# Kernel tuning notes

Hardware: AMD Instinct MI355X
Metric: run time of the kernel (lower is better)

The kernel has to match this reference:

```python
import jax, jax.numpy as jnp
import numpy as np

EMBED_DIM = 512
U_EMBED = 6
NUM_HEADS = 8
HEAD_DIM = EMBED_DIM // NUM_HEADS
SCALE = HEAD_DIM ** -0.5
BS, N = 8, 1024


def setup_inputs() -> dict:
    key = jax.random.key(0)
    ks = jax.random.split(key, 9)
    x = jax.random.normal(ks[0], (BS, N, EMBED_DIM), dtype=jnp.float32)
    u = jax.random.normal(ks[1], (BS, U_EMBED, N, N), dtype=jnp.float32)
    umask = jax.random.randint(ks[2], (BS, N, N, 1), 0, 2).astype(bool)
    s = EMBED_DIM ** -0.5
    Wq = jax.random.normal(ks[3], (EMBED_DIM, EMBED_DIM), dtype=jnp.float32) * s
    Wk = jax.random.normal(ks[4], (EMBED_DIM, EMBED_DIM), dtype=jnp.float32) * s
    Wv = jax.random.normal(ks[5], (EMBED_DIM, EMBED_DIM), dtype=jnp.float32) * s
    Wu = jax.random.normal(ks[6], (NUM_HEADS, U_EMBED), dtype=jnp.float32) * (U_EMBED ** -0.5)
    bu = jnp.zeros((NUM_HEADS,), dtype=jnp.float32)
    Wo = jax.random.normal(ks[7], (EMBED_DIM, EMBED_DIM), dtype=jnp.float32) * s
    bo = jnp.zeros((EMBED_DIM,), dtype=jnp.float32)
    return {"x": x, "u": u, "umask": umask, "Wq": Wq, "Wk": Wk, "Wv": Wv,
            "Wu": Wu, "bu": bu, "Wo": Wo, "bo": bo}


def reference(x, u, umask, Wq, Wk, Wv, Wu, bu, Wo, bo):
    bs, n, _ = x.shape
    # projections (torch Linear: y = x @ W.T)
    Q = (x @ Wq.T).reshape(bs, n, NUM_HEADS, HEAD_DIM)
    K = (x @ Wk.T).reshape(bs, n, NUM_HEADS, HEAD_DIM)
    V = (x @ Wv.T).reshape(bs, n, NUM_HEADS, HEAD_DIM)
    # scores: [bs, H, N, N]
    scores = jnp.einsum('bqhd,bkhd->bhqk', Q, K) * SCALE
    # 1x1 conv bias: [bs, u_embed, N, N] -> [bs, H, N, N]
    ub = jnp.einsum('bunm,hu->bhnm', u, Wu) + bu[None, :, None, None]
    # umask: [bs, N, N, 1] -> transpose(3,1) -> [bs, 1, N, N]
    m = jnp.transpose(umask, (0, 3, 2, 1))
    ub = jnp.where(m, -jnp.inf, ub)
    scores = scores + ub
    attn = jax.nn.softmax(scores, axis=-1)
    ctx = jnp.einsum('bhqk,bkhd->bqhd', attn, V).reshape(bs, n, EMBED_DIM)
    out = ctx @ Wo.T + bo
    return out, attn
```

## Files before the change

kernel.cpp:

```cpp
#include <hip/hip_runtime.h>
#include <hip/hip_bf16.h>
#include <math.h>

#define BSZ 8
#define SEQ 1024
#define EMB 512
#define NH 8
#define HD 64
#define UE 6
#define QKSCALE 0.125f

typedef unsigned short u16;
typedef short bf16x8 __attribute__((ext_vector_type(8)));
typedef float f32x4 __attribute__((ext_vector_type(4)));
typedef unsigned short ushort4_t __attribute__((ext_vector_type(4)));

__device__ __forceinline__ u16 f2bf(float f) {
  unsigned u = __float_as_uint(f);
  unsigned r = (u + 0x7fffu + ((u >> 16) & 1u)) >> 16;
  return (u16)r;
}
__device__ __forceinline__ void f2hl(float f, u16& hi, u16& lo) {
  hi = f2bf(f);
  float fh = __uint_as_float(((unsigned)hi) << 16);
  lo = f2bf(f - fh);
}
#define F2HL_V(fv, hv, lv, idx)            \
  {                                        \
    u16 _h, _l;                            \
    f2hl((fv), _h, _l);                    \
    (hv)[idx] = (short)_h;                 \
    (lv)[idx] = (short)_l;                 \
  }
__device__ __forceinline__ f32x4 mfma_bf16(bf16x8 a, bf16x8 b, f32x4 c) {
  return __builtin_amdgcn_mfma_f32_16x16x32_bf16(a, b, c, 0, 0, 0);
}

__global__ __launch_bounds__(256) void split_kernel(const float* __restrict__ src,
                                                    u16* __restrict__ hi, u16* __restrict__ lo, int n4) {
  int i = blockIdx.x * 256 + threadIdx.x;
  if (i >= n4) return;
  float4 v = ((const float4*)src)[i];
  ushort4_t h, l;
  F2HL_V(v.x, h, l, 0); F2HL_V(v.y, h, l, 1);
  F2HL_V(v.z, h, l, 2); F2HL_V(v.w, h, l, 3);
  ((ushort4_t*)hi)[i] = h;
  ((ushort4_t*)lo)[i] = l;
}

__global__ __launch_bounds__(256, 2) void qkv_mfma_kernel(
    const float* __restrict__ x, const u16* __restrict__ Wsp,
    u16* __restrict__ Qhi, u16* __restrict__ Qlo,
    u16* __restrict__ Khi, u16* __restrict__ Klo, u16* __restrict__ Vt) {
  const int mt = blockIdx.x, h = blockIdx.y, wsel = blockIdx.z;
  const int m0 = mt * 64, c0 = h * 64;
  const u16* __restrict__ WH = Wsp + (size_t)wsel * 524288;
  const u16* __restrict__ WL = WH + 262144;
  __shared__ u16 AH[64][40], AL[64][40], BH[64][40], BL[64][40];
  __shared__ u16 vout[64][69];
  const int t = threadIdx.x, w = t >> 6, l = t & 63;
  const int wr = (w >> 1) * 32, wc = (w & 1) * 32;
  f32x4 acc[2][2] = {};
  const int srow = t >> 2;
  for (int e0 = 0; e0 < EMB; e0 += 32) {
    {
      const int c = (t & 3) * 8;
      float4 v0 = *(const float4*)&x[(size_t)(m0 + srow) * EMB + e0 + c];
      float4 v1 = *(const float4*)&x[(size_t)(m0 + srow) * EMB + e0 + c + 4];
      ushort4_t h0, l0, h1, l1;
      F2HL_V(v0.x, h0, l0, 0); F2HL_V(v0.y, h0, l0, 1); F2HL_V(v0.z, h0, l0, 2); F2HL_V(v0.w, h0, l0, 3);
      F2HL_V(v1.x, h1, l1, 0); F2HL_V(v1.y, h1, l1, 1); F2HL_V(v1.z, h1, l1, 2); F2HL_V(v1.w, h1, l1, 3);
      *(ushort4_t*)&AH[srow][c] = h0; *(ushort4_t*)&AH[srow][c + 4] = h1;
      *(ushort4_t*)&AL[srow][c] = l0; *(ushort4_t*)&AL[srow][c + 4] = l1;
      *(bf16x8*)&BH[srow][c] = *(const bf16x8*)&WH[(size_t)(c0 + srow) * EMB + e0 + c];
      *(bf16x8*)&BL[srow][c] = *(const bf16x8*)&WL[(size_t)(c0 + srow) * EMB + e0 + c];
    }
    __syncthreads();
    const int ar = l & 15, ach = (l >> 4) << 3;
    bf16x8 ah0 = *(bf16x8*)&AH[wr + ar][ach],      ah1 = *(bf16x8*)&AH[wr + 16 + ar][ach];
    bf16x8 al0 = *(bf16x8*)&AL[wr + ar][ach],      al1 = *(bf16x8*)&AL[wr + 16 + ar][ach];
    bf16x8 bh0 = *(bf16x8*)&BH[wc + ar][ach],      bh1 = *(bf16x8*)&BH[wc + 16 + ar][ach];
    bf16x8 bl0 = *(bf16x8*)&BL[wc + ar][ach],      bl1 = *(bf16x8*)&BL[wc + 16 + ar][ach];
    acc[0][0] = mfma_bf16(ah0, bh0, acc[0][0]); acc[0][0] = mfma_bf16(ah0, bl0, acc[0][0]); acc[0][0] = mfma_bf16(al0, bh0, acc[0][0]);
    acc[0][1] = mfma_bf16(ah0, bh1, acc[0][1]); acc[0][1] = mfma_bf16(ah0, bl1, acc[0][1]); acc[0][1] = mfma_bf16(al0, bh1, acc[0][1]);
    acc[1][0] = mfma_bf16(ah1, bh0, acc[1][0]); acc[1][0] = mfma_bf16(ah1, bl0, acc[1][0]); acc[1][0] = mfma_bf16(al1, bh0, acc[1][0]);
    acc[1][1] = mfma_bf16(ah1, bh1, acc[1][1]); acc[1][1] = mfma_bf16(ah1, bl1, acc[1][1]); acc[1][1] = mfma_bf16(al1, bh1, acc[1][1]);
    __syncthreads();
  }
  const int bb = m0 >> 10, n0 = m0 & 1023;
  if (wsel < 2) {
    u16* __restrict__ OH = wsel ? Khi : Qhi;
    u16* __restrict__ OL = wsel ? Klo : Qlo;
#pragma unroll
    for (int i = 0; i < 2; ++i)
#pragma unroll
      for (int j = 0; j < 2; ++j) {
        const int col = wc + 16 * j + (l & 15);
#pragma unroll
        for (int r = 0; r < 4; ++r) {
          const int n = n0 + wr + 16 * i + ((l >> 4) << 2) + r;
          size_t o = ((size_t)(bb * NH + h) * SEQ + n) * HD + col;
          u16 hi, lo; f2hl(acc[i][j][r], hi, lo);
          OH[o] = hi; OL[o] = lo;
        }
      }
  } else {
#pragma unroll
    for (int i = 0; i < 2; ++i)
#pragma unroll
      for (int j = 0; j < 2; ++j) {
        const int col = wc + 16 * j + (l & 15);
#pragma unroll
        for (int r = 0; r < 4; ++r)
          vout[wr + 16 * i + ((l >> 4) << 2) + r][col] = f2bf(acc[i][j][r]);
      }
    __syncthreads();
    const int d = t >> 2, nch = (t & 3) * 16;
    bf16x8 o0, o1;
#pragma unroll
    for (int i = 0; i < 8; ++i) o0[i] = (short)vout[nch + i][d];
#pragma unroll
    for (int i = 0; i < 8; ++i) o1[i] = (short)vout[nch + 8 + i][d];
    size_t dst = ((size_t)(bb * NH + h) * HD + d) * SEQ + n0 + nch;
    *(bf16x8*)&Vt[dst] = o0;
    *(bf16x8*)&Vt[dst + 8] = o1;
  }
}

__global__ __launch_bounds__(256, 2) void scores_kernel(
    const u16* __restrict__ Qhi, const u16* __restrict__ Qlo,
    const u16* __restrict__ Khi, const u16* __restrict__ Klo,
    const float* __restrict__ u, const int* __restrict__ umask,
    const float* __restrict__ Wu, const float* __restrict__ bu,
    float* __restrict__ attn, float* __restrict__ sums) {
  const int kt = blockIdx.x, qt = blockIdx.y, b = blockIdx.z;
  const int q0 = qt * 64, k0 = kt * 64;
  __shared__ u16 KsH[2][64][68], KsL[2][64][68];
  __shared__ unsigned char ms[64][68];
  const int t = threadIdx.x, w = t >> 6, l = t & 63;
  const int kl = l & 15, g = l >> 4;
  const int qb = 16 * w + (g << 2);

#pragma unroll
  for (int r = 0; r < 16; ++r) {
    int idx = r * 256 + t; int k = idx >> 6, q = idx & 63;
    ms[k][q] = (unsigned char)(umask[((size_t)b * SEQ + k0 + k) * SEQ + q0 + q] != 0);
  }

  unsigned upk[UE][4][2];
  const float* ubase = u + ((size_t)b * UE * SEQ + q0 + qb) * SEQ + k0 + kl;
#pragma unroll
  for (int uu = 0; uu < UE; ++uu)
#pragma unroll
    for (int tt = 0; tt < 4; ++tt)
#pragma unroll
      for (int p = 0; p < 2; ++p) {
        const float* up = ubase + (size_t)uu * SEQ * SEQ + (size_t)(2 * p) * SEQ + 16 * tt;
        upk[uu][tt][p] = (unsigned)f2bf(up[0]) | ((unsigned)f2bf(up[SEQ]) << 16);
      }

  const int krow_s = t >> 2, kc_s = (t & 3) * 16;
  bf16x8 preH[2][2], preL[2][2];
#pragma unroll
  for (int h2 = 0; h2 < 2; ++h2) {
    const u16* kp = Khi + ((size_t)(b * NH + h2) * SEQ + k0 + krow_s) * HD + kc_s;
    const u16* kq = Klo + ((size_t)(b * NH + h2) * SEQ + k0 + krow_s) * HD + kc_s;
    preH[h2][0] = *(const bf16x8*)kp; preH[h2][1] = *(const bf16x8*)(kp + 8);
    preL[h2][0] = *(const bf16x8*)kq; preL[h2][1] = *(const bf16x8*)(kq + 8);
  }

  for (int hp = 0; hp < 4; ++hp) {
    const int h0 = hp * 2;
    __syncthreads();
#pragma unroll
    for (int h2 = 0; h2 < 2; ++h2) {
      *(bf16x8*)&KsH[h2][krow_s][kc_s] = preH[h2][0];
      *(bf16x8*)&KsH[h2][krow_s][kc_s + 8] = preH[h2][1];
      *(bf16x8*)&KsL[h2][krow_s][kc_s] = preL[h2][0];
      *(bf16x8*)&KsL[h2][krow_s][kc_s + 8] = preL[h2][1];
    }
    if (hp < 3) {
#pragma unroll
      for (int h2 = 0; h2 < 2; ++h2) {
        const u16* kp = Khi + ((size_t)(b * NH + h0 + 2 + h2) * SEQ + k0 + krow_s) * HD + kc_s;
        const u16* kq = Klo + ((size_t)(b * NH + h0 + 2 + h2) * SEQ + k0 + krow_s) * HD + kc_s;
        preH[h2][0] = *(const bf16x8*)kp; preH[h2][1] = *(const bf16x8*)(kp + 8);
        preL[h2][0] = *(const bf16x8*)kq; preL[h2][1] = *(const bf16x8*)(kq + 8);
      }
    }
    __syncthreads();

    bf16x8 qh[2][2], qo[2][2];
    float wu_[2][UE], bub[2];
    float* abase[2];
#pragma unroll
    for (int h2 = 0; h2 < 2; ++h2) {
      const int bh = b * NH + h0 + h2;
      const u16* qp = Qhi + ((size_t)bh * SEQ + q0 + 16 * w + kl) * HD + (g << 3);
      const u16* qq = Qlo + ((size_t)bh * SEQ + q0 + 16 * w + kl) * HD + (g << 3);
      qh[h2][0] = *(const bf16x8*)qp; qh[h2][1] = *(const bf16x8*)(qp + 32);
      qo[h2][0] = *(const bf16x8*)qq; qo[h2][1] = *(const bf16x8*)(qq + 32);
#pragma unroll
      for (int uu = 0; uu < UE; ++uu) wu_[h2][uu] = Wu[(h0 + h2) * UE + uu];
      bub[h2] = bu[h0 + h2];
      abase[h2] = attn + ((size_t)bh * SEQ + q0 + qb) * SEQ + k0 + kl;
    }

    float esum[2][4] = {};
#pragma unroll
    for (int tt = 0; tt < 4; ++tt) {
      const int krow = tt * 16 + kl, kch = g << 3;
      bf16x8 kh00 = *(bf16x8*)&KsH[0][krow][kch], kh01 = *(bf16x8*)&KsH[0][krow][kch + 32];
      bf16x8 kb00 = *(bf16x8*)&KsL[0][krow][kch], kb01 = *(bf16x8*)&KsL[0][krow][kch + 32];
      bf16x8 kh10 = *(bf16x8*)&KsH[1][krow][kch], kh11 = *(bf16x8*)&KsH[1][krow][kch + 32];
      bf16x8 kb10 = *(bf16x8*)&KsL[1][krow][kch], kb11 = *(bf16x8*)&KsL[1][krow][kch + 32];
      f32x4 a0 = {0.f, 0.f, 0.f, 0.f}, a1 = {0.f, 0.f, 0.f, 0.f};
      a0 = mfma_bf16(qh[0][0], kh00, a0);  a1 = mfma_bf16(qh[1][0], kh10, a1);
      a0 = mfma_bf16(qh[0][1], kh01, a0);  a1 = mfma_bf16(qh[1][1], kh11, a1);
      a0 = mfma_bf16(qh[0][0], kb00, a0);  a1 = mfma_bf16(qh[1][0], kb10, a1);
      a0 = mfma_bf16(qh[0][1], kb01, a0);  a1 = mfma_bf16(qh[1][1], kb11, a1);
      a0 = mfma_bf16(qo[0][0], kh00, a0);  a1 = mfma_bf16(qo[1][0], kh10, a1);
      a0 = mfma_bf16(qo[0][1], kh01, a0);  a1 = mfma_bf16(qo[1][1], kh11, a1);
#pragma unroll
      for (int p = 0; p < 2; ++p) {
        float ub0x = bub[0], ub0y = bub[0], ub1x = bub[1], ub1y = bub[1];
#pragma unroll
        for (int uu = 0; uu < UE; ++uu) {
          unsigned pk = upk[uu][tt][p];
          float flo = __uint_as_float(pk << 16);
          float fhi = __uint_as_float(pk & 0xffff0000u);
          ub0x = fmaf(wu_[0][uu], flo, ub0x); ub0y = fmaf(wu_[0][uu], fhi, ub0y);
          ub1x = fmaf(wu_[1][uu], flo, ub1x); ub1y = fmaf(wu_[1][uu], fhi, ub1y);
        }
        const unsigned char m0 = ms[tt * 16 + kl][qb + 2 * p];
        const unsigned char m1 = ms[tt * 16 + kl][qb + 2 * p + 1];
        float v00 = a0[2 * p] * QKSCALE + ub0x, v01 = a0[2 * p + 1] * QKSCALE + ub0y;
        float v10 = a1[2 * p] * QKSCALE + ub1x, v11 = a1[2 * p + 1] * QKSCALE + ub1y;
        abase[0][(size_t)(2 * p) * SEQ + tt * 16]     = m0 ? -INFINITY : v00;
        abase[0][(size_t)(2 * p + 1) * SEQ + tt * 16] = m1 ? -INFINITY : v01;
        abase[1][(size_t)(2 * p) * SEQ + tt * 16]     = m0 ? -INFINITY : v10;
        abase[1][(size_t)(2 * p + 1) * SEQ + tt * 16] = m1 ? -INFINITY : v11;
        esum[0][2 * p]     += m0 ? 0.f : __expf(v00);
        esum[0][2 * p + 1] += m1 ? 0.f : __expf(v01);
        esum[1][2 * p]     += m0 ? 0.f : __expf(v10);
        esum[1][2 * p + 1] += m1 ? 0.f : __expf(v11);
      }
    }
#pragma unroll
    for (int h2 = 0; h2 < 2; ++h2)
#pragma unroll
      for (int r = 0; r < 4; ++r) {
#pragma unroll
        for (int o = 1; o <= 8; o <<= 1) esum[h2][r] += __shfl_xor(esum[h2][r], o);
      }
    if (kl == 0) {
#pragma unroll
      for (int h2 = 0; h2 < 2; ++h2)
#pragma unroll
        for (int r = 0; r < 4; ++r)
          sums[((size_t)(b * NH + h0 + h2) * SEQ + q0 + qb + r) * 16 + kt] = esum[h2][r];
    }
  }
}

__global__ __launch_bounds__(256, 2) void pv_softmax_kernel(
    float* __restrict__ attn, const u16* __restrict__ Vt,
    const float* __restrict__ sums, u16* __restrict__ ctx) {
  const int qt = blockIdx.x, bh = blockIdx.y;
  const int q0 = qt * 64;
  __shared__ u16 Pl[64][72], Vs[64][72];
  const int t = threadIdx.x, w = t >> 6, l = t & 63;
  const int row = t >> 2, cc = (t & 3) * 16;
  float* arow = attn + ((size_t)bh * SEQ + q0 + row) * SEQ + cc;

  float S = 0.f;
  {
    const float* sp = sums + ((size_t)bh * SEQ + q0 + row) * 16 + (t & 3) * 4;
#pragma unroll
    for (int j = 0; j < 4; ++j) S += sp[j];
#pragma unroll
    for (int o = 1; o <= 2; o <<= 1) S += __shfl_xor(S, o);
  }
  const float inv = 1.0f / S;

  const int wr = (w >> 1) * 32, wc = (w & 1) * 32;
  f32x4 acc[2][2] = {};
  float4 va0 = *(const float4*)(arow + 0), va1 = *(const float4*)(arow + 4);
  float4 va2 = *(const float4*)(arow + 8), va3 = *(const float4*)(arow + 12);
  const u16* vrow = Vt + ((size_t)bh * HD + row) * SEQ + cc;
  bf16x8 vb0 = *(const bf16x8*)vrow, vb1 = *(const bf16x8*)(vrow + 8);

  for (int k0 = 0; k0 < SEQ; k0 += 64) {
    bf16x8 p0, p1;
    float4 p;
    p.x = __expf(va0.x) * inv; p.y = __expf(va0.y) * inv;
    p.z = __expf(va0.z) * inv; p.w = __expf(va0.w) * inv;
    *(float4*)(arow + k0 + 0) = p;
    p0[0] = (short)f2bf(p.x); p0[1] = (short)f2bf(p.y); p0[2] = (short)f2bf(p.z); p0[3] = (short)f2bf(p.w);
    p.x = __expf(va1.x) * inv; p.y = __expf(va1.y) * inv;
    p.z = __expf(va1.z) * inv; p.w = __expf(va1.w) * inv;
    *(float4*)(arow + k0 + 4) = p;
    p0[4] = (short)f2bf(p.x); p0[5] = (short)f2bf(p.y); p0[6] = (short)f2bf(p.z); p0[7] = (short)f2bf(p.w);
    p.x = __expf(va2.x) * inv; p.y = __expf(va2.y) * inv;
    p.z = __expf(va2.z) * inv; p.w = __expf(va2.w) * inv;
    *(float4*)(arow + k0 + 8) = p;
    p1[0] = (short)f2bf(p.x); p1[1] = (short)f2bf(p.y); p1[2] = (short)f2bf(p.z); p1[3] = (short)f2bf(p.w);
    p.x = __expf(va3.x) * inv; p.y = __expf(va3.y) * inv;
    p.z = __expf(va3.z) * inv; p.w = __expf(va3.w) * inv;
    *(float4*)(arow + k0 + 12) = p;
    p1[4] = (short)f2bf(p.x); p1[5] = (short)f2bf(p.y); p1[6] = (short)f2bf(p.z); p1[7] = (short)f2bf(p.w);

    *(bf16x8*)&Pl[row][cc] = p0;
    *(bf16x8*)&Pl[row][cc + 8] = p1;
    *(bf16x8*)&Vs[row][cc] = vb0;
    *(bf16x8*)&Vs[row][cc + 8] = vb1;

    if (k0 + 64 < SEQ) {
      va0 = *(const float4*)(arow + k0 + 64);
      va1 = *(const float4*)(arow + k0 + 68);
      va2 = *(const float4*)(arow + k0 + 72);
      va3 = *(const float4*)(arow + k0 + 76);
      vb0 = *(const bf16x8*)(vrow + k0 + 64);
      vb1 = *(const bf16x8*)(vrow + k0 + 72);
    }
    __syncthreads();
#pragma unroll
    for (int kb = 0; kb < 2; ++kb) {
      const int kch = kb * 32 + ((l >> 4) << 3);
      bf16x8 a0 = *(bf16x8*)&Pl[wr + (l & 15)][kch];
      bf16x8 a1 = *(bf16x8*)&Pl[wr + 16 + (l & 15)][kch];
      bf16x8 b0 = *(bf16x8*)&Vs[wc + (l & 15)][kch];
      bf16x8 b1 = *(bf16x8*)&Vs[wc + 16 + (l & 15)][kch];
      acc[0][0] = mfma_bf16(a0, b0, acc[0][0]);
      acc[0][1] = mfma_bf16(a0, b1, acc[0][1]);
      acc[1][0] = mfma_bf16(a1, b0, acc[1][0]);
      acc[1][1] = mfma_bf16(a1, b1, acc[1][1]);
    }
    __syncthreads();
  }
  const int b = bh >> 3, h = bh & 7;
#pragma unroll
  for (int i = 0; i < 2; ++i)
#pragma unroll
    for (int j = 0; j < 2; ++j) {
      const int d = h * HD + wc + 16 * j + (l & 15);
#pragma unroll
      for (int r = 0; r < 4; ++r) {
        const int q = q0 + wr + 16 * i + ((l >> 4) << 2) + r;
        ctx[((size_t)(b * SEQ + q)) * EMB + d] = f2bf(acc[i][j][r]);
      }
    }
}

__global__ __launch_bounds__(256, 2) void oproj_kernel(
    const u16* __restrict__ ctx,
    const u16* __restrict__ WoH, const u16* __restrict__ WoL,
    const float* __restrict__ bo, float* __restrict__ out) {
  const int mt = blockIdx.x, ct = blockIdx.y;
  const int m0 = mt * 64, c0 = ct * 64;
  __shared__ u16 AH[64][40], BH[64][40], BL[64][40];
  const int t = threadIdx.x, w = t >> 6, l = t & 63;
  const int wr = (w >> 1) * 32, wc = (w & 1) * 32;
  f32x4 acc[2][2] = {};
  const int srow = t >> 2, sc = (t & 3) * 8;
  for (int e0 = 0; e0 < EMB; e0 += 32) {
    *(bf16x8*)&AH[srow][sc] = *(const bf16x8*)&ctx[(size_t)(m0 + srow) * EMB + e0 + sc];
    *(bf16x8*)&BH[srow][sc] = *(const bf16x8*)&WoH[(size_t)(c0 + srow) * EMB + e0 + sc];
    *(bf16x8*)&BL[srow][sc] = *(const bf16x8*)&WoL[(size_t)(c0 + srow) * EMB + e0 + sc];
    __syncthreads();
    const int ar = l & 15, ach = (l >> 4) << 3;
    bf16x8 ah0 = *(bf16x8*)&AH[wr + ar][ach],      ah1 = *(bf16x8*)&AH[wr + 16 + ar][ach];
    bf16x8 bh0 = *(bf16x8*)&BH[wc + ar][ach],      bh1 = *(bf16x8*)&BH[wc + 16 + ar][ach];
    bf16x8 bl0 = *(bf16x8*)&BL[wc + ar][ach],      bl1 = *(bf16x8*)&BL[wc + 16 + ar][ach];
    acc[0][0] = mfma_bf16(ah0, bh0, acc[0][0]); acc[0][0] = mfma_bf16(ah0, bl0, acc[0][0]);
    acc[0][1] = mfma_bf16(ah0, bh1, acc[0][1]); acc[0][1] = mfma_bf16(ah0, bl1, acc[0][1]);
    acc[1][0] = mfma_bf16(ah1, bh0, acc[1][0]); acc[1][0] = mfma_bf16(ah1, bl0, acc[1][0]);
    acc[1][1] = mfma_bf16(ah1, bh1, acc[1][1]); acc[1][1] = mfma_bf16(ah1, bl1, acc[1][1]);
    __syncthreads();
  }
#pragma unroll
  for (int i = 0; i < 2; ++i)
#pragma unroll
    for (int j = 0; j < 2; ++j) {
      const int col = c0 + wc + 16 * j + (l & 15);
      const float bias = bo[col];
#pragma unroll
      for (int r = 0; r < 4; ++r) {
        const int m = m0 + wr + 16 * i + ((l >> 4) << 2) + r;
        out[(size_t)m * EMB + col] = acc[i][j][r] + bias;
      }
    }
}

extern "C" void kernel_launch(void* const* d_in, const int* in_sizes, int n_in,
                              void* d_out, int out_size, void* d_ws, size_t ws_size,
                              hipStream_t stream) {
  const float* x = (const float*)d_in[0];
  const float* u = (const float*)d_in[1];
  const int* umask = (const int*)d_in[2];
  const float* Wq = (const float*)d_in[3];
  const float* Wk = (const float*)d_in[4];
  const float* Wv = (const float*)d_in[5];
  const float* Wu = (const float*)d_in[6];
  const float* bu = (const float*)d_in[7];
  const float* Wo = (const float*)d_in[8];
  const float* bo = (const float*)d_in[9];

  float* out = (float*)d_out;
  float* attn = out + (size_t)BSZ * SEQ * EMB;

  const size_t per = (size_t)BSZ * NH * SEQ * HD;
  u16* ws = (u16*)d_ws;
  u16* Qhi = ws;
  u16* Qlo = Qhi + per;
  u16* Khi = Qlo + per;
  u16* Klo = Khi + per;
  u16* Vt = Klo + per;
  u16* ctx = Vt + per;
  float* sums = (float*)(ctx + per);
  u16* Wsp = (u16*)(sums + (size_t)BSZ * NH * SEQ * 16);

  const int wn4 = 262144 / 4;
  split_kernel<<<dim3(wn4 / 256), 256, 0, stream>>>(Wq, Wsp + 0 * 524288, Wsp + 0 * 524288 + 262144, wn4);
  split_kernel<<<dim3(wn4 / 256), 256, 0, stream>>>(Wk, Wsp + 1 * 524288, Wsp + 1 * 524288 + 262144, wn4);
  split_kernel<<<dim3(wn4 / 256), 256, 0, stream>>>(Wv, Wsp + 2 * 524288, Wsp + 2 * 524288 + 262144, wn4);
  split_kernel<<<dim3(wn4 / 256), 256, 0, stream>>>(Wo, Wsp + 3 * 524288, Wsp + 3 * 524288 + 262144, wn4);

  qkv_mfma_kernel<<<dim3(128, 8, 3), 256, 0, stream>>>(x, Wsp, Qhi, Qlo, Khi, Klo, Vt);
  scores_kernel<<<dim3(16, 16, 8), 256, 0, stream>>>(Qhi, Qlo, Khi, Klo, u, umask, Wu, bu, attn, sums);
  pv_softmax_kernel<<<dim3(16, 64), 256, 0, stream>>>(attn, Vt, sums, ctx);
  oproj_kernel<<<dim3(128, 8), 256, 0, stream>>>(ctx, Wsp + 3 * 524288, Wsp + 3 * 524288 + 262144, bo, out);
}
```

Before: 395.2 us.

## Store unnormalized bf16 exp scores in attn buffer and defer normalization

The scores kernel now writes exp(score) as bf16 into the upper half of each fp32 attn row instead of raw fp32 scores. The softmax/PV kernel reads these bf16 values, writes the normalized fp32 attn, feeds them straight into the MFMA, and applies 1/sum to ctx at the end. The aim is to halve the intermediate write and read traffic on the large attention tensor and drop the second exp pass. x is also pre-split into hi/lo bf16 once, using the attn buffer as scratch, instead of in every qkv block. Exp values are rounded to bf16 before summing, so the stored attention loses precision compared with the fp32 path. The in-place aliasing only works because each row writes output columns ahead of the bf16 region it is still reading.

Measured after the change: 430.4 us. +8.9%, slower.

```diff
diff --git a/kernel.cpp b/kernel.cpp
--- a/kernel.cpp
+++ b/kernel.cpp
@@ -19,6 +19,9 @@
   unsigned u = __float_as_uint(f);
   unsigned r = (u + 0x7fffu + ((u >> 16) & 1u)) >> 16;
   return (u16)r;
+}
+__device__ __forceinline__ float bf2f(u16 v) {
+  return __uint_as_float(((unsigned)v) << 16);
 }
 __device__ __forceinline__ void f2hl(float f, u16& hi, u16& lo) {
   hi = f2bf(f);
@@ -49,7 +52,7 @@
 }
 
 __global__ __launch_bounds__(256, 2) void qkv_mfma_kernel(
-    const float* __restrict__ x, const u16* __restrict__ Wsp,
+    const u16* __restrict__ Xhi, const u16* __restrict__ Xlo, const u16* __restrict__ Wsp,
     u16* __restrict__ Qhi, u16* __restrict__ Qlo,
     u16* __restrict__ Khi, u16* __restrict__ Klo, u16* __restrict__ Vt) {
   const int mt = blockIdx.x, h = blockIdx.y, wsel = blockIdx.z;
@@ -65,13 +68,8 @@
   for (int e0 = 0; e0 < EMB; e0 += 32) {
     {
       const int c = (t & 3) * 8;
-      float4 v0 = *(const float4*)&x[(size_t)(m0 + srow) * EMB + e0 + c];
-      float4 v1 = *(const float4*)&x[(size_t)(m0 + srow) * EMB + e0 + c + 4];
-      ushort4_t h0, l0, h1, l1;
-      F2HL_V(v0.x, h0, l0, 0); F2HL_V(v0.y, h0, l0, 1); F2HL_V(v0.z, h0, l0, 2); F2HL_V(v0.w, h0, l0, 3);
-      F2HL_V(v1.x, h1, l1, 0); F2HL_V(v1.y, h1, l1, 1); F2HL_V(v1.z, h1, l1, 2); F2HL_V(v1.w, h1, l1, 3);
-      *(ushort4_t*)&AH[srow][c] = h0; *(ushort4_t*)&AH[srow][c + 4] = h1;
-      *(ushort4_t*)&AL[srow][c] = l0; *(ushort4_t*)&AL[srow][c + 4] = l1;
+      *(bf16x8*)&AH[srow][c] = *(const bf16x8*)&Xhi[(size_t)(m0 + srow) * EMB + e0 + c];
+      *(bf16x8*)&AL[srow][c] = *(const bf16x8*)&Xlo[(size_t)(m0 + srow) * EMB + e0 + c];
       *(bf16x8*)&BH[srow][c] = *(const bf16x8*)&WH[(size_t)(c0 + srow) * EMB + e0 + c];
       *(bf16x8*)&BL[srow][c] = *(const bf16x8*)&WL[(size_t)(c0 + srow) * EMB + e0 + c];
     }
@@ -132,7 +130,7 @@
     const u16* __restrict__ Khi, const u16* __restrict__ Klo,
     const float* __restrict__ u, const int* __restrict__ umask,
     const float* __restrict__ Wu, const float* __restrict__ bu,
-    float* __restrict__ attn, float* __restrict__ sums) {
+    u16* __restrict__ praw, float* __restrict__ sums) {
   const int kt = blockIdx.x, qt = blockIdx.y, b = blockIdx.z;
   const int q0 = qt * 64, k0 = kt * 64;
   __shared__ u16 KsH[2][64][68], KsL[2][64][68];
@@ -192,7 +190,7 @@
 
     bf16x8 qh[2][2], qo[2][2];
     float wu_[2][UE], bub[2];
-    float* abase[2];
+    u16* pbase[2];
 #pragma unroll
     for (int h2 = 0; h2 < 2; ++h2) {
       const int bh = b * NH + h0 + h2;
@@ -203,7 +201,7 @@
 #pragma unroll
       for (int uu = 0; uu < UE; ++uu) wu_[h2][uu] = Wu[(h0 + h2) * UE + uu];
       bub[h2] = bu[h0 + h2];
-      abase[h2] = attn + ((size_t)bh * SEQ + q0 + qb) * SEQ + k0 + kl;
+      pbase[h2] = praw + ((size_t)(bh * SEQ + q0 + qb)) * 2048 + 1024 + k0 + kl;
     }
 
     float esum[2][4] = {};
@@ -234,16 +232,18 @@
         }
         const unsigned char m0 = ms[tt * 16 + kl][qb + 2 * p];
         const unsigned char m1 = ms[tt * 16 + kl][qb + 2 * p + 1];
-        float v00 = a0[2 * p] * QKSCALE + ub0x, v01 = a0[2 * p + 1] * QKSCALE + ub0y;
-        float v10 = a1[2 * p] * QKSCALE + ub1x, v11 = a1[2 * p + 1] * QKSCALE + ub1y;
-        abase[0][(size_t)(2 * p) * SEQ + tt * 16]     = m0 ? -INFINITY : v00;
-        abase[0][(size_t)(2 * p + 1) * SEQ + tt * 16] = m1 ? -INFINITY : v01;
-        abase[1][(size_t)(2 * p) * SEQ + tt * 16]     = m0 ? -INFINITY : v10;
-        abase[1][(size_t)(2 * p + 1) * SEQ + tt * 16] = m1 ? -INFINITY : v11;
-        esum[0][2 * p]     += m0 ? 0.f : __expf(v00);
-        esum[0][2 * p + 1] += m1 ? 0.f : __expf(v01);
-        esum[1][2 * p]     += m0 ? 0.f : __expf(v10);
-        esum[1][2 * p + 1] += m1 ? 0.f : __expf(v11);
+        u16 e00 = m0 ? (u16)0 : f2bf(__expf(a0[2 * p] * QKSCALE + ub0x));
+        u16 e01 = m1 ? (u16)0 : f2bf(__expf(a0[2 * p + 1] * QKSCALE + ub0y));
+        u16 e10 = m0 ? (u16)0 : f2bf(__expf(a1[2 * p] * QKSCALE + ub1x));
+        u16 e11 = m1 ? (u16)0 : f2bf(__expf(a1[2 * p + 1] * QKSCALE + ub1y));
+        pbase[0][(size_t)(2 * p) * 2048 + tt * 16]     = e00;
+        pbase[0][(size_t)(2 * p + 1) * 2048 + tt * 16] = e01;
+        pbase[1][(size_t)(2 * p) * 2048 + tt * 16]     = e10;
+        pbase[1][(size_t)(2 * p + 1) * 2048 + tt * 16] = e11;
+        esum[0][2 * p]     += bf2f(e00);
+        esum[0][2 * p + 1] += bf2f(e01);
+        esum[1][2 * p]     += bf2f(e10);
+        esum[1][2 * p + 1] += bf2f(e11);
       }
     }
 #pragma unroll
@@ -263,15 +263,15 @@
   }
 }
 
-__global__ __launch_bounds__(256, 2) void pv_softmax_kernel(
-    float* __restrict__ attn, const u16* __restrict__ Vt,
+__global__ __launch_bounds__(256, 4) void pv_softmax_kernel(
+    float* attn, const u16* __restrict__ Vt,
     const float* __restrict__ sums, u16* __restrict__ ctx) {
   const int qt = blockIdx.x, bh = blockIdx.y;
   const int q0 = qt * 64;
   __shared__ u16 Pl[64][72], Vs[64][72];
+  __shared__ float invl[64];
   const int t = threadIdx.x, w = t >> 6, l = t & 63;
   const int row = t >> 2, cc = (t & 3) * 16;
-  float* arow = attn + ((size_t)bh * SEQ + q0 + row) * SEQ + cc;
 
   float S = 0.f;
   {
@@ -282,44 +282,40 @@
     for (int o = 1; o <= 2; o <<= 1) S += __shfl_xor(S, o);
   }
   const float inv = 1.0f / S;
+  if ((t & 3) == 0) invl[row] = inv;
+
+  const u16* prow = (const u16*)attn + ((size_t)(bh * SEQ + q0 + row)) * 2048 + 1024;
+  float* arow = attn + ((size_t)(bh * SEQ + q0 + row)) * SEQ;
+  const u16* vrow = Vt + ((size_t)bh * HD + row) * SEQ + cc;
 
   const int wr = (w >> 1) * 32, wc = (w & 1) * 32;
   f32x4 acc[2][2] = {};
-  float4 va0 = *(const float4*)(arow + 0), va1 = *(const float4*)(arow + 4);
-  float4 va2 = *(const float4*)(arow + 8), va3 = *(const float4*)(arow + 12);
-  const u16* vrow = Vt + ((size_t)bh * HD + row) * SEQ + cc;
+  bf16x8 pa = *(const bf16x8*)&prow[cc], pb = *(const bf16x8*)&prow[cc + 8];
   bf16x8 vb0 = *(const bf16x8*)vrow, vb1 = *(const bf16x8*)(vrow + 8);
 
   for (int k0 = 0; k0 < SEQ; k0 += 64) {
-    bf16x8 p0, p1;
-    float4 p;
-    p.x = __expf(va0.x) * inv; p.y = __expf(va0.y) * inv;
-    p.z = __expf(va0.z) * inv; p.w = __expf(va0.w) * inv;
-    *(float4*)(arow + k0 + 0) = p;
-    p0[0] = (short)f2bf(p.x); p0[1] = (short)f2bf(p.y); p0[2] = (short)f2bf(p.z); p0[3] = (short)f2bf(p.w);
-    p.x = __expf(va1.x) * inv; p.y = __expf(va1.y) * inv;
-    p.z = __expf(va1.z) * inv; p.w = __expf(va1.w) * inv;
-    *(float4*)(arow + k0 + 4) = p;
-    p0[4] = (short)f2bf(p.x); p0[5] = (short)f2bf(p.y); p0[6] = (short)f2bf(p.z); p0[7] = (short)f2bf(p.w);
-    p.x = __expf(va2.x) * inv; p.y = __expf(va2.y) * inv;
-    p.z = __expf(va2.z) * inv; p.w = __expf(va2.w) * inv;
-    *(float4*)(arow + k0 + 8) = p;
-    p1[0] = (short)f2bf(p.x); p1[1] = (short)f2bf(p.y); p1[2] = (short)f2bf(p.z); p1[3] = (short)f2bf(p.w);
-    p.x = __expf(va3.x) * inv; p.y = __expf(va3.y) * inv;
-    p.z = __expf(va3.z) * inv; p.w = __expf(va3.w) * inv;
-    *(float4*)(arow + k0 + 12) = p;
-    p1[4] = (short)f2bf(p.x); p1[5] = (short)f2bf(p.y); p1[6] = (short)f2bf(p.z); p1[7] = (short)f2bf(p.w);
-
-    *(bf16x8*)&Pl[row][cc] = p0;
-    *(bf16x8*)&Pl[row][cc + 8] = p1;
+    float* ap = arow + k0 + cc;
+    {
+      float4 o0, o1, o2, o3;
+      o0.x = bf2f((u16)pa[0]) * inv; o0.y = bf2f((u16)pa[1]) * inv;
+      o0.z = bf2f((u16)pa[2]) * inv; o0.w = bf2f((u16)pa[3]) * inv;
+      o1.x = bf2f((u16)pa[4]) * inv; o1.y = bf2f((u16)pa[5]) * inv;
+      o1.z = bf2f((u16)pa[6]) * inv; o1.w = bf2f((u16)pa[7]) * inv;
+      o2.x = bf2f((u16)pb[0]) * inv; o2.y = bf2f((u16)pb[1]) * inv;
+      o2.z = bf2f((u16)pb[2]) * inv; o2.w = bf2f((u16)pb[3]) * inv;
+      o3.x = bf2f((u16)pb[4]) * inv; o3.y = bf2f((u16)pb[5]) * inv;
+      o3.z = bf2f((u16)pb[6]) * inv; o3.w = bf2f((u16)pb[7]) * inv;
+      ((float4*)ap)[0] = o0; ((float4*)ap)[1] = o1;
+      ((float4*)ap)[2] = o2; ((float4*)ap)[3] = o3;
+    }
+    *(bf16x8*)&Pl[row][cc] = pa;
+    *(bf16x8*)&Pl[row][cc + 8] = pb;
     *(bf16x8*)&Vs[row][cc] = vb0;
     *(bf16x8*)&Vs[row][cc + 8] = vb1;
 
     if (k0 + 64 < SEQ) {
-      va0 = *(const float4*)(arow + k0 + 64);
-      va1 = *(const float4*)(arow + k0 + 68);
-      va2 = *(const float4*)(arow + k0 + 72);
-      va3 = *(const float4*)(arow + k0 + 76);
+      pa = *(const bf16x8*)&prow[k0 + 64 + cc];
+      pb = *(const bf16x8*)&prow[k0 + 64 + cc + 8];
       vb0 = *(const bf16x8*)(vrow + k0 + 64);
       vb1 = *(const bf16x8*)(vrow + k0 + 72);
     }
@@ -346,8 +342,8 @@
       const int d = h * HD + wc + 16 * j + (l & 15);
 #pragma unroll
       for (int r = 0; r < 4; ++r) {
-        const int q = q0 + wr + 16 * i + ((l >> 4) << 2) + r;
-        ctx[((size_t)(b * SEQ + q)) * EMB + d] = f2bf(acc[i][j][r]);
+        const int ql_ = wr + 16 * i + ((l >> 4) << 2) + r;
+        ctx[((size_t)(b * SEQ + q0 + ql_)) * EMB + d] = f2bf(acc[i][j][r] * invl[ql_]);
       }
     }
 }
@@ -420,14 +416,20 @@
   float* sums = (float*)(ctx + per);
   u16* Wsp = (u16*)(sums + (size_t)BSZ * NH * SEQ * 16);
 
+  u16* Xhi = (u16*)attn;
+  u16* Xlo = Xhi + (size_t)BSZ * SEQ * EMB;
+
   const int wn4 = 262144 / 4;
   split_kernel<<<dim3(wn4 / 256), 256, 0, stream>>>(Wq, Wsp + 0 * 524288, Wsp + 0 * 524288 + 262144, wn4);
   split_kernel<<<dim3(wn4 / 256), 256, 0, stream>>>(Wk, Wsp + 1 * 524288, Wsp + 1 * 524288 + 262144, wn4);
   split_kernel<<<dim3(wn4 / 256), 256, 0, stream>>>(Wv, Wsp + 2 * 524288, Wsp + 2 * 524288 + 262144, wn4);
   split_kernel<<<dim3(wn4 / 256), 256, 0, stream>>>(Wo, Wsp + 3 * 524288, Wsp + 3 * 524288 + 262144, wn4);
-
-  qkv_mfma_kernel<<<dim3(128, 8, 3), 256, 0, stream>>>(x, Wsp, Qhi, Qlo, Khi, Klo, Vt);
-  scores_kernel<<<dim3(16, 16, 8), 256, 0, stream>>>(Qhi, Qlo, Khi, Klo, u, umask, Wu, bu, attn, sums);
+  const int xn4 = (int)((size_t)BSZ * SEQ * EMB / 4);
+  split_kernel<<<dim3(xn4 / 256), 256, 0, stream>>>(x, Xhi, Xlo, xn4);
+
+  qkv_mfma_kernel<<<dim3(128, 8, 3), 256, 0, stream>>>(Xhi, Xlo, Wsp, Qhi, Qlo, Khi, Klo, Vt);
+  scores_kernel<<<dim3(16, 16, 8), 256, 0, stream>>>(Qhi, Qlo, Khi, Klo, u, umask, Wu, bu,
+                                                     (u16*)attn, sums);
   pv_softmax_kernel<<<dim3(16, 64), 256, 0, stream>>>(attn, Vt, sums, ctx);
   oproj_kernel<<<dim3(128, 8), 256, 0, stream>>>(ctx, Wsp + 3 * 524288, Wsp + 3 * 524288 + 262144, bo, out);
 }
```
